# Kernel optimization log

Hardware: AMD Instinct MI355X
Metric: run time of the kernel (lower is better)

The kernel has to match this reference:

```python
import jax, jax.numpy as jnp
import numpy as np

HEAD_SIZE = 64
NUM_HEADS = 8
D_IN = 512

def setup_inputs() -> dict:
    key = jax.random.key(0)
    ks = jax.random.split(key, 6)
    B, Nq, Nk = 4, 2048, 2048
    HD = HEAD_SIZE * NUM_HEADS
    q = jax.random.normal(ks[0], (B, Nq, D_IN), dtype=jnp.float32)
    k = jax.random.normal(ks[1], (B, Nk, D_IN), dtype=jnp.float32)
    s = 1.0 / np.sqrt(D_IN)
    Wq = jax.random.normal(ks[2], (D_IN, HD), dtype=jnp.float32) * s
    Wk = jax.random.normal(ks[3], (D_IN, HD), dtype=jnp.float32) * s
    Wv = jax.random.normal(ks[4], (D_IN, HD), dtype=jnp.float32) * s
    Wh = jax.random.normal(ks[5], (HD, HEAD_SIZE), dtype=jnp.float32) * (1.0 / np.sqrt(HD))
    return {"q": q, "k": k, "Wq": Wq, "Wk": Wk, "Wv": Wv, "Wh": Wh}

def reference(q, k, Wq, Wk, Wv, Wh):
    B, Nq, _ = q.shape
    Nk = k.shape[1]
    H, hs = NUM_HEADS, HEAD_SIZE
    # QKV projections (no bias), reshape to [B, H, N, hs]
    q_ = (q @ Wq).reshape(B, Nq, H, hs).transpose(0, 2, 1, 3)
    k_ = (k @ Wk).reshape(B, Nk, H, hs).transpose(0, 2, 1, 3)
    v_ = (k @ Wv).reshape(B, Nk, H, hs).transpose(0, 2, 1, 3)
    scale = 1.0 / jnp.sqrt(jnp.float32(hs))
    score = jnp.einsum('bhqd,bhkd->bhqk', q_, k_) * scale  # [B,H,Nq,Nk]
    attn = jax.nn.softmax(score, axis=-1)
    wv = jnp.einsum('bhqk,bhkd->bhqd', attn, v_)  # [B,H,Nq,hs]
    wv = wv.transpose(0, 2, 1, 3).reshape(B, Nq, H * hs)
    return wv @ Wh  # [B, Nq, hs]
```

## Files before the change

kernel.cpp:

```cpp
#include <hip/hip_runtime.h>
#include <hip/hip_bf16.h>

#define BB   4
#define NQ   2048
#define NKK  2048
#define DIN  512
#define NH   8
#define HS   64
#define HD   512

typedef __hip_bfloat16 bf16;
typedef unsigned short ushort_t;
typedef __attribute__((ext_vector_type(8))) short short8;
typedef __attribute__((ext_vector_type(4))) float f32x4;
typedef __attribute__((ext_vector_type(16))) float f32x16;
typedef __attribute__((ext_vector_type(4))) unsigned u32x4;

__device__ __forceinline__ unsigned short f2bu(float x) {
  bf16 h = __float2bfloat16(x);
  return *(unsigned short*)&h;
}

__global__ __launch_bounds__(256) void wtrans_kernel(
    const float* __restrict__ Wq, const float* __restrict__ Wk,
    const float* __restrict__ Wv, const float* __restrict__ Wh,
    ushort_t* __restrict__ Wt, ushort_t* __restrict__ Wht) {
  const int z = blockIdx.z;
  const float* src;
  ushort_t* dst;
  int S;
  if (z < 3) {
    src = (z == 0) ? Wq : (z == 1) ? Wk : Wv;
    dst = Wt + (size_t)z * 512 * 512;
    S = 512;
  } else {
    if (blockIdx.y != 0) return;
    src = Wh;
    dst = Wht;
    S = 64;
  }
  const int k0 = blockIdx.x * 64;
  const int n0 = (z < 3) ? blockIdx.y * 64 : 0;

  __shared__ ushort_t Ls[64 * 72];
  const int tid = threadIdx.x;
  {
    int r = tid >> 2, cb = (tid & 3) * 16;
    const float* sp = src + (size_t)(k0 + r) * S + n0 + cb;
#pragma unroll
    for (int ii = 0; ii < 4; ++ii) {
      float4 f = *(const float4*)(sp + ii * 4);
      __align__(8) ushort_t t4[4] = {f2bu(f.x), f2bu(f.y), f2bu(f.z), f2bu(f.w)};
      *(uint2*)(&Ls[r * 72 + cb + ii * 4]) = *(uint2*)t4;
    }
  }
  __syncthreads();
  {
    int rr = tid >> 2, tb = (tid & 3) * 16;
    __align__(16) ushort_t tmp[16];
#pragma unroll
    for (int j = 0; j < 16; ++j) tmp[j] = Ls[(tb + j) * 72 + rr];
    ushort_t* dp = dst + (size_t)(n0 + rr) * 512 + k0 + tb;
    *(int4*)dp       = ((int4*)tmp)[0];
    *(int4*)(dp + 8) = ((int4*)tmp)[1];
  }
}

__global__ __launch_bounds__(256) void proj_kernel(
    const float* __restrict__ q, const float* __restrict__ k,
    const ushort_t* __restrict__ Wt, ushort_t* __restrict__ Qf,
    ushort_t* __restrict__ Kf, ushort_t* __restrict__ Vt) {
  const int z = blockIdx.y;
  const float* X = (z == 0) ? q : k;
  const ushort_t* Wz = Wt + (size_t)z * 512 * 512;
  const float sc = (z == 0) ? 0.18033688011112042f : 1.0f;

  __shared__ ushort_t Xs[64 * 520];

  const int tid  = threadIdx.x;
  const int lane = tid & 63;
  const int w    = tid >> 6;
  const int quad = lane >> 4;
  const int c    = lane & 15;

  const int m0 = blockIdx.x * 64;

  {
    const int r  = tid >> 2;
    const int c4 = (tid & 3) * 4;
    const float* xp = X + (size_t)(m0 + r) * DIN;
    ushort_t* lp = &Xs[r * 520];
#pragma unroll
    for (int i = 0; i < 32; ++i) {
      const int col = c4 + i * 16;
      float4 f = *(const float4*)(xp + col);
      __align__(8) ushort_t t4[4] = {f2bu(f.x), f2bu(f.y), f2bu(f.z), f2bu(f.w)};
      *(uint2*)(lp + col) = *(uint2*)t4;
    }
  }
  __syncthreads();

  const int n0w = w * 128;

  f32x4 acc[4][8];
#pragma unroll
  for (int m = 0; m < 4; ++m)
#pragma unroll
    for (int n = 0; n < 8; ++n) acc[m][n] = (f32x4)0.0f;

#pragma unroll 2
  for (int ks = 0; ks < 16; ++ks) {
    short8 af[4];
#pragma unroll
    for (int m = 0; m < 4; ++m)
      af[m] = *(const short8*)(&Xs[(m * 16 + c) * 520 + ks * 32 + quad * 8]);
#pragma unroll
    for (int n = 0; n < 8; ++n) {
      short8 bn = *(const short8*)(Wz + (size_t)(n0w + n * 16 + c) * 512 +
                                   ks * 32 + quad * 8);
#pragma unroll
      for (int m = 0; m < 4; ++m)
        acc[m][n] = __builtin_amdgcn_mfma_f32_16x16x32_bf16(af[m], bn, acc[m][n], 0, 0, 0);
    }
  }

  if (z == 2) {
#pragma unroll
    for (int m = 0; m < 4; ++m)
#pragma unroll
      for (int n = 0; n < 8; ++n) {
        const int row0 = m0 + m * 16 + quad * 4;
        const int col  = n0w + n * 16 + c;
        const int bb   = row0 >> 11;
        const int t0   = row0 & 2047;
        __align__(8) ushort_t t4[4] = {f2bu(acc[m][n][0]), f2bu(acc[m][n][1]),
                                       f2bu(acc[m][n][2]), f2bu(acc[m][n][3])};
        *(uint2*)(&Vt[((size_t)bb * HD + col) * NKK + t0]) = *(uint2*)t4;
      }
  } else {
    ushort_t* Y = (z == 0) ? Qf : Kf;
#pragma unroll
    for (int m = 0; m < 4; ++m)
#pragma unroll
      for (int n = 0; n < 8; ++n)
#pragma unroll
        for (int r = 0; r < 4; ++r) {
          const int row = m0 + m * 16 + quad * 4 + r;
          const int col = n0w + n * 16 + c;
          Y[(size_t)row * HD + col] = f2bu(acc[m][n][r] * sc);
        }
  }
}

__global__ __launch_bounds__(64, 1) void attn_kernel(
    const ushort_t* __restrict__ Qf, const ushort_t* __restrict__ Kf,
    const ushort_t* __restrict__ Vt, ushort_t* __restrict__ CTX) {
  const int id   = blockIdx.x;
  const int xcd  = id & 7;
  const int slot = id >> 3;
  const int p    = xcd * 4 + (slot >> 5);
  const int qb   = slot & 31;
  const int h    = p & 7;
  const int b    = p >> 3;

  __shared__ ushort_t Kt[2][4096];
  __shared__ ushort_t Vs[2][4096];

  const int lane = threadIdx.x & 63;
  const int ql   = lane & 31;
  const int hi   = lane >> 5;

  const int q0 = qb * 64;

  short8 bq[2][4];
#pragma unroll
  for (int qs = 0; qs < 2; ++qs) {
    const ushort_t* qp =
        Qf + (size_t)(b * NQ + q0 + qs * 32 + ql) * HD + h * HS + hi * 8;
#pragma unroll
    for (int ks = 0; ks < 4; ++ks) bq[qs][ks] = *(const short8*)(qp + ks * 16);
  }

  const int sub  = lane >> 3;
  const int slt  = lane & 7;
  const int csrc = slt ^ sub;
  const ushort_t* kp0 =
      Kf + (size_t)(b * NKK + sub) * HD + h * HS + csrc * 8;
  const ushort_t* vp0 =
      Vt + (size_t)((b * NH + h) * HS + sub) * NKK + csrc * 8;

  auto stage = [&](int buf, int kt) {
    const ushort_t* kp = kp0 + (size_t)kt * 64 * HD;
    const ushort_t* vp = vp0 + (size_t)kt * 64;
#pragma unroll
    for (int i = 0; i < 8; ++i) {
      __builtin_amdgcn_global_load_lds(
          (const __attribute__((address_space(1))) unsigned*)(kp + (size_t)i * 8 * HD),
          (__attribute__((address_space(3))) unsigned*)(&Kt[buf][i * 512]),
          16, 0, 0);
      __builtin_amdgcn_global_load_lds(
          (const __attribute__((address_space(1))) unsigned*)(vp + (size_t)i * 8 * NKK),
          (__attribute__((address_space(3))) unsigned*)(&Vs[buf][i * 512]),
          16, 0, 0);
    }
  };

  f32x16 o[2][2];
#pragma unroll
  for (int qs = 0; qs < 2; ++qs)
#pragma unroll
    for (int ng = 0; ng < 2; ++ng) o[qs][ng] = (f32x16)0.0f;
  float lsum[2] = {0.0f, 0.0f};

  stage(0, 0);

  for (int t = 0; t < NKK / 64; ++t) {
    const int buf = t & 1;
    if (t < NKK / 64 - 1) {
      stage(buf ^ 1, t + 1);
      asm volatile("s_waitcnt vmcnt(16)" ::: "memory");
    } else {
      asm volatile("s_waitcnt vmcnt(0)" ::: "memory");
    }
    const ushort_t* kb = &Kt[buf][0];
    const ushort_t* vb = &Vs[buf][0];

    short8 ak[2][4], bv[2][4];
#pragma unroll
    for (int kg = 0; kg < 2; ++kg) {
      const int krow = kg * 32 + ql;
#pragma unroll
      for (int ks = 0; ks < 4; ++ks)
        ak[kg][ks] = *(const short8*)(&kb[krow * 64 + (((ks * 2 + hi) ^ (krow & 7)) * 8)]);
    }
#pragma unroll
    for (int ng = 0; ng < 2; ++ng) {
      const int vrow = ng * 32 + ql;
#pragma unroll
      for (int ks = 0; ks < 4; ++ks)
        bv[ng][ks] = *(const short8*)(&vb[vrow * 64 + (((ks * 2 + hi) ^ (vrow & 7)) * 8)]);
    }

#pragma unroll
    for (int kg = 0; kg < 2; ++kg) {
      f32x16 s[2];
      s[0] = (f32x16)0.0f;
      s[1] = (f32x16)0.0f;
#pragma unroll
      for (int ks = 0; ks < 4; ++ks) {
        s[0] = __builtin_amdgcn_mfma_f32_32x32x16_bf16(ak[kg][ks], bq[0][ks], s[0], 0, 0, 0);
        s[1] = __builtin_amdgcn_mfma_f32_32x32x16_bf16(ak[kg][ks], bq[1][ks], s[1], 0, 0, 0);
      }

      short8 pa[2][2];
#pragma unroll
      for (int qs = 0; qs < 2; ++qs) {
        float p_[16];
#pragma unroll
        for (int r = 0; r < 16; ++r) p_[r] = __builtin_amdgcn_exp2f(s[qs][r]);
        {
          float a0 = p_[0] + p_[1], a1 = p_[2] + p_[3], a2 = p_[4] + p_[5], a3 = p_[6] + p_[7];
          float a4 = p_[8] + p_[9], a5 = p_[10] + p_[11], a6 = p_[12] + p_[13], a7 = p_[14] + p_[15];
          a0 += a1; a2 += a3; a4 += a5; a6 += a7;
          lsum[qs] += (a0 + a2) + (a4 + a6);
        }
#pragma unroll
        for (int sp = 0; sp < 2; ++sp) {
          unsigned wA, wB, wC, wD;
          asm("v_cvt_pk_bf16_f32 %0, %1, %2" : "=v"(wA) : "v"(p_[8 * sp + 0]), "v"(p_[8 * sp + 1]));
          asm("v_cvt_pk_bf16_f32 %0, %1, %2" : "=v"(wB) : "v"(p_[8 * sp + 2]), "v"(p_[8 * sp + 3]));
          asm("v_cvt_pk_bf16_f32 %0, %1, %2" : "=v"(wC) : "v"(p_[8 * sp + 4]), "v"(p_[8 * sp + 5]));
          asm("v_cvt_pk_bf16_f32 %0, %1, %2" : "=v"(wD) : "v"(p_[8 * sp + 6]), "v"(p_[8 * sp + 7]));
          asm("v_permlane32_swap_b32 %0, %1" : "+v"(wA), "+v"(wC));
          asm("v_permlane32_swap_b32 %0, %1" : "+v"(wB), "+v"(wD));
          u32x4 pw;
          pw.x = wA;
          pw.y = wB;
          pw.z = wC;
          pw.w = wD;
          pa[qs][sp] = __builtin_bit_cast(short8, pw);
        }
      }

#pragma unroll
      for (int sp = 0; sp < 2; ++sp) {
        const int ks = kg * 2 + sp;
#pragma unroll
        for (int ng = 0; ng < 2; ++ng) {
          o[0][ng] = __builtin_amdgcn_mfma_f32_32x32x16_bf16(pa[0][sp], bv[ng][ks], o[0][ng], 0, 0, 0);
          o[1][ng] = __builtin_amdgcn_mfma_f32_32x32x16_bf16(pa[1][sp], bv[ng][ks], o[1][ng], 0, 0, 0);
        }
      }
    }
  }

  float inv[2];
#pragma unroll
  for (int qs = 0; qs < 2; ++qs) {
    float tot = lsum[qs] + __shfl_xor(lsum[qs], 32);
    inv[qs] = 1.0f / tot;
  }

#pragma unroll
  for (int qs = 0; qs < 2; ++qs)
#pragma unroll
    for (int r = 0; r < 16; ++r) {
      int qr = (r & 3) + 8 * (r >> 2) + 4 * hi;
      float iv = __shfl(inv[qs], qr);
      size_t base = (size_t)(b * NQ + q0 + qs * 32 + qr) * HD + h * HS + ql;
      CTX[base]      = f2bu(o[qs][0][r] * iv);
      CTX[base + 32] = f2bu(o[qs][1][r] * iv);
    }
}

__global__ __launch_bounds__(64) void outproj_kernel(
    const ushort_t* __restrict__ CTX, const ushort_t* __restrict__ Wht,
    float* __restrict__ out) {
  const int lane = threadIdx.x & 63;
  const int quad = lane >> 4, c = lane & 15;
  const int m0 = blockIdx.x * 16;

  f32x4 o[4];
#pragma unroll
  for (int n = 0; n < 4; ++n) o[n] = (f32x4)0.0f;

  const ushort_t* arow = CTX + (size_t)(m0 + c) * HD;
#pragma unroll 4
  for (int ks = 0; ks < 16; ++ks) {
    short8 a = *(const short8*)(arow + ks * 32 + quad * 8);
#pragma unroll
    for (int nd = 0; nd < 4; ++nd) {
      short8 bn = *(const short8*)(Wht + (size_t)(nd * 16 + c) * 512 + ks * 32 + quad * 8);
      o[nd] = __builtin_amdgcn_mfma_f32_16x16x32_bf16(a, bn, o[nd], 0, 0, 0);
    }
  }
#pragma unroll
  for (int nd = 0; nd < 4; ++nd)
#pragma unroll
    for (int r = 0; r < 4; ++r)
      out[(size_t)(m0 + quad * 4 + r) * HS + nd * 16 + c] = o[nd][r];
}

extern "C" void kernel_launch(void* const* d_in, const int* in_sizes, int n_in,
                              void* d_out, int out_size, void* d_ws,
                              size_t ws_size, hipStream_t stream) {
  const float* q  = (const float*)d_in[0];
  const float* k  = (const float*)d_in[1];
  const float* Wq = (const float*)d_in[2];
  const float* Wk = (const float*)d_in[3];
  const float* Wv = (const float*)d_in[4];
  const float* Wh = (const float*)d_in[5];
  float* out = (float*)d_out;

  const size_t E = (size_t)BB * NQ * HD;
  ushort_t* ws  = (ushort_t*)d_ws;
  ushort_t* Qf  = ws;
  ushort_t* Kf  = Qf + E;
  ushort_t* Vt  = Kf + E;
  ushort_t* CTX = Vt + E;
  ushort_t* Vf  = CTX + E;
  ushort_t* Wt  = Vf + E;
  ushort_t* Wht = Wt + (size_t)3 * 512 * 512;

  wtrans_kernel<<<dim3(8, 8, 4), 256, 0, stream>>>(Wq, Wk, Wv, Wh, Wt, Wht);
  proj_kernel<<<dim3(BB * NQ / 64, 3), 256, 0, stream>>>(
      q, k, Wt, Qf, Kf, Vt);
  attn_kernel<<<dim3(32 * NH * BB), 64, 0, stream>>>(Qf, Kf, Vt, CTX);
  outproj_kernel<<<dim3(BB * NQ / 16), 64, 0, stream>>>(CTX, Wht, out);
}
```

Measured before the change: 204.3 us.

## Pre-swizzle projection weights into MFMA fragment order and halve proj row tile

The weight transpose kernel now writes Wq/Wk/Wv in a pre-tiled layout where each lane's 8-element B fragment for a 32-wide k-slice and 16-column block is contiguous. The projection kernel can then load B fragments with fully coalesced 16-byte loads instead of strided row reads. The projection tile also shrinks from 64 to 32 rows per block, doubling the grid and lowering register and LDS use for better occupancy, at the cost of more weight re-reads per output row.

```diff
diff --git a/kernel.cpp b/kernel.cpp
--- a/kernel.cpp
+++ b/kernel.cpp
@@ -25,44 +25,64 @@
     const float* __restrict__ Wq, const float* __restrict__ Wk,
     const float* __restrict__ Wv, const float* __restrict__ Wh,
     ushort_t* __restrict__ Wt, ushort_t* __restrict__ Wht) {
+  __shared__ ushort_t Ls[4608];
+  const int tid = threadIdx.x;
   const int z = blockIdx.z;
-  const float* src;
-  ushort_t* dst;
-  int S;
-  if (z < 3) {
-    src = (z == 0) ? Wq : (z == 1) ? Wk : Wv;
-    dst = Wt + (size_t)z * 512 * 512;
-    S = 512;
-  } else {
-    if (blockIdx.y != 0) return;
-    src = Wh;
-    dst = Wht;
-    S = 64;
-  }
-  const int k0 = blockIdx.x * 64;
-  const int n0 = (z < 3) ? blockIdx.y * 64 : 0;
-
-  __shared__ ushort_t Ls[64 * 72];
-  const int tid = threadIdx.x;
+
+  if (z == 3) {
+    if (blockIdx.y != 0 || blockIdx.x >= 8) return;
+    const int k0 = blockIdx.x * 64;
+    {
+      int r = tid >> 2, cb = (tid & 3) * 16;
+      const float* sp = Wh + (size_t)(k0 + r) * 64 + cb;
+#pragma unroll
+      for (int ii = 0; ii < 4; ++ii) {
+        float4 f = *(const float4*)(sp + ii * 4);
+        __align__(8) ushort_t t4[4] = {f2bu(f.x), f2bu(f.y), f2bu(f.z), f2bu(f.w)};
+        *(uint2*)(&Ls[r * 72 + cb + ii * 4]) = *(uint2*)t4;
+      }
+    }
+    __syncthreads();
+    {
+      int rr = tid >> 2, tb = (tid & 3) * 16;
+      __align__(16) ushort_t tmp[16];
+#pragma unroll
+      for (int j = 0; j < 16; ++j) tmp[j] = Ls[(tb + j) * 72 + rr];
+      ushort_t* dp = Wht + (size_t)rr * 512 + k0 + tb;
+      *(int4*)dp       = ((int4*)tmp)[0];
+      *(int4*)(dp + 8) = ((int4*)tmp)[1];
+    }
+    return;
+  }
+
+  const int ks = blockIdx.x;
+  const int nc = blockIdx.y;
+  const float* src = (z == 0) ? Wq : (z == 1) ? Wk : Wv;
   {
-    int r = tid >> 2, cb = (tid & 3) * 16;
-    const float* sp = src + (size_t)(k0 + r) * S + n0 + cb;
+    int kk = tid >> 3;
+    int c0 = (tid & 7) * 16;
+    const float* sp = src + (size_t)(ks * 32 + kk) * 512 + nc * 128 + c0;
 #pragma unroll
     for (int ii = 0; ii < 4; ++ii) {
       float4 f = *(const float4*)(sp + ii * 4);
       __align__(8) ushort_t t4[4] = {f2bu(f.x), f2bu(f.y), f2bu(f.z), f2bu(f.w)};
-      *(uint2*)(&Ls[r * 72 + cb + ii * 4]) = *(uint2*)t4;
+      *(uint2*)(&Ls[kk * 136 + c0 + ii * 4]) = *(uint2*)t4;
     }
   }
   __syncthreads();
   {
-    int rr = tid >> 2, tb = (tid & 3) * 16;
-    __align__(16) ushort_t tmp[16];
-#pragma unroll
-    for (int j = 0; j < 16; ++j) tmp[j] = Ls[(tb + j) * 72 + rr];
-    ushort_t* dp = dst + (size_t)(n0 + rr) * 512 + k0 + tb;
-    *(int4*)dp       = ((int4*)tmp)[0];
-    *(int4*)(dp + 8) = ((int4*)tmp)[1];
+    ushort_t* dst = Wt + (((size_t)z * 4 + nc) * 16 + ks) * 4096;
+#pragma unroll
+    for (int f2 = 0; f2 < 2; ++f2) {
+      const int f  = tid * 2 + f2;
+      const int n  = f >> 6;
+      const int lo = f & 63;
+      const int cc = lo & 15, qq = lo >> 4;
+      __align__(16) ushort_t tmp[8];
+#pragma unroll
+      for (int j = 0; j < 8; ++j) tmp[j] = Ls[(qq * 8 + j) * 136 + n * 16 + cc];
+      *(int4*)(dst + f * 8) = *(int4*)tmp;
+    }
   }
 }
 
@@ -72,10 +92,9 @@
     ushort_t* __restrict__ Kf, ushort_t* __restrict__ Vt) {
   const int z = blockIdx.y;
   const float* X = (z == 0) ? q : k;
-  const ushort_t* Wz = Wt + (size_t)z * 512 * 512;
   const float sc = (z == 0) ? 0.18033688011112042f : 1.0f;
 
-  __shared__ ushort_t Xs[64 * 520];
+  __shared__ ushort_t Xs[32 * 524];
 
   const int tid  = threadIdx.x;
   const int lane = tid & 63;
@@ -83,16 +102,16 @@
   const int quad = lane >> 4;
   const int c    = lane & 15;
 
-  const int m0 = blockIdx.x * 64;
+  const int m0 = blockIdx.x * 32;
 
   {
-    const int r  = tid >> 2;
-    const int c4 = (tid & 3) * 4;
+    const int r  = tid >> 3;
+    const int c0 = (tid & 7) * 4;
     const float* xp = X + (size_t)(m0 + r) * DIN;
-    ushort_t* lp = &Xs[r * 520];
-#pragma unroll
-    for (int i = 0; i < 32; ++i) {
-      const int col = c4 + i * 16;
+    ushort_t* lp = &Xs[r * 524];
+#pragma unroll
+    for (int i = 0; i < 16; ++i) {
+      const int col = c0 + i * 32;
       float4 f = *(const float4*)(xp + col);
       __align__(8) ushort_t t4[4] = {f2bu(f.x), f2bu(f.y), f2bu(f.z), f2bu(f.w)};
       *(uint2*)(lp + col) = *(uint2*)t4;
@@ -100,37 +119,34 @@
   }
   __syncthreads();
 
-  const int n0w = w * 128;
-
-  f32x4 acc[4][8];
-#pragma unroll
-  for (int m = 0; m < 4; ++m)
+  const ushort_t* Wz = Wt + (((size_t)z * 4 + w) * 16) * 4096 + lane * 8;
+
+  f32x4 acc[2][8];
+#pragma unroll
+  for (int m = 0; m < 2; ++m)
 #pragma unroll
     for (int n = 0; n < 8; ++n) acc[m][n] = (f32x4)0.0f;
 
-#pragma unroll 2
+#pragma unroll 4
   for (int ks = 0; ks < 16; ++ks) {
-    short8 af[4];
-#pragma unroll
-    for (int m = 0; m < 4; ++m)
-      af[m] = *(const short8*)(&Xs[(m * 16 + c) * 520 + ks * 32 + quad * 8]);
+    short8 af0 = *(const short8*)(&Xs[c * 524 + ks * 32 + quad * 8]);
+    short8 af1 = *(const short8*)(&Xs[(16 + c) * 524 + ks * 32 + quad * 8]);
+    const ushort_t* wk = Wz + (size_t)ks * 4096;
 #pragma unroll
     for (int n = 0; n < 8; ++n) {
-      short8 bn = *(const short8*)(Wz + (size_t)(n0w + n * 16 + c) * 512 +
-                                   ks * 32 + quad * 8);
-#pragma unroll
-      for (int m = 0; m < 4; ++m)
-        acc[m][n] = __builtin_amdgcn_mfma_f32_16x16x32_bf16(af[m], bn, acc[m][n], 0, 0, 0);
+      short8 bn = *(const short8*)(wk + n * 512);
+      acc[0][n] = __builtin_amdgcn_mfma_f32_16x16x32_bf16(af0, bn, acc[0][n], 0, 0, 0);
+      acc[1][n] = __builtin_amdgcn_mfma_f32_16x16x32_bf16(af1, bn, acc[1][n], 0, 0, 0);
     }
   }
 
   if (z == 2) {
 #pragma unroll
-    for (int m = 0; m < 4; ++m)
+    for (int m = 0; m < 2; ++m)
 #pragma unroll
       for (int n = 0; n < 8; ++n) {
         const int row0 = m0 + m * 16 + quad * 4;
-        const int col  = n0w + n * 16 + c;
+        const int col  = w * 128 + n * 16 + c;
         const int bb   = row0 >> 11;
         const int t0   = row0 & 2047;
         __align__(8) ushort_t t4[4] = {f2bu(acc[m][n][0]), f2bu(acc[m][n][1]),
@@ -140,13 +156,13 @@
   } else {
     ushort_t* Y = (z == 0) ? Qf : Kf;
 #pragma unroll
-    for (int m = 0; m < 4; ++m)
+    for (int m = 0; m < 2; ++m)
 #pragma unroll
       for (int n = 0; n < 8; ++n)
 #pragma unroll
         for (int r = 0; r < 4; ++r) {
           const int row = m0 + m * 16 + quad * 4 + r;
-          const int col = n0w + n * 16 + c;
+          const int col = w * 128 + n * 16 + c;
           Y[(size_t)row * HD + col] = f2bu(acc[m][n][r] * sc);
         }
   }
@@ -362,8 +378,8 @@
   ushort_t* Wt  = Vf + E;
   ushort_t* Wht = Wt + (size_t)3 * 512 * 512;
 
-  wtrans_kernel<<<dim3(8, 8, 4), 256, 0, stream>>>(Wq, Wk, Wv, Wh, Wt, Wht);
-  proj_kernel<<<dim3(BB * NQ / 64, 3), 256, 0, stream>>>(
+  wtrans_kernel<<<dim3(16, 4, 4), 256, 0, stream>>>(Wq, Wk, Wv, Wh, Wt, Wht);
+  proj_kernel<<<dim3(BB * NQ / 32, 3), 256, 0, stream>>>(
       q, k, Wt, Qf, Kf, Vt);
   attn_kernel<<<dim3(32 * NH * BB), 64, 0, stream>>>(Qf, Kf, Vt, CTX);
   outproj_kernel<<<dim3(BB * NQ / 16), 64, 0, stream>>>(CTX, Wht, out);
```

New measurement: 167.4 us (median of 2 runs). 1.22x faster.
